# Optimization experiments

Measured on AMD Instinct MI355X. Metric: run time of the kernel, lower is better.

## Reference

```python
import math
import jax, jax.numpy as jnp
import numpy as np


def positionalencoding1d(d_model, length):
    # [length, d_model]; d_model must be even
    position = jnp.arange(length, dtype=jnp.float32)[:, None]
    div_term = jnp.exp(jnp.arange(0, d_model, 2, dtype=jnp.float32) * (-(math.log(10000.0) / d_model)))
    pe = jnp.zeros((length, d_model), dtype=jnp.float32)
    pe = pe.at[:, 0::2].set(jnp.sin(position * div_term))
    pe = pe.at[:, 1::2].set(jnp.cos(position * div_term))
    return pe


def setup_inputs() -> dict:
    key = jax.random.key(0)
    k1, k2, k3 = jax.random.split(key, 3)
    B, D, H, W = 64, 512, 32, 32
    NH = 8
    DH = D // NH
    x = jax.random.normal(k1, (B, D, H, W), dtype=jnp.float32)
    q = jax.random.normal(k2, (1, NH, 1, DH), dtype=jnp.float32)
    Wkv = jax.random.normal(k3, (D, 2 * D), dtype=jnp.float32) * 0.02
    bkv = jnp.zeros((2 * D,), dtype=jnp.float32)
    return {"x": x, "q": q, "Wkv": Wkv, "bkv": bkv, "num_heads": NH}


def reference(x, q, Wkv, bkv, num_heads):
    B, d, h, w = x.shape
    N = h * w
    NH = num_heads
    DH = d // NH
    scale = DH ** (-0.5)

    xt = x.reshape(B, d, N).transpose(0, 2, 1)            # b n d
    kv = xt @ Wkv + bkv                                   # b n 2d
    k, v = jnp.split(kv, 2, axis=-1)
    k = k.reshape(B, N, NH, DH).transpose(0, 2, 1, 3)     # b h n d
    v = v.reshape(B, N, NH, DH).transpose(0, 2, 1, 3)     # b h n d

    pe = positionalencoding1d(DH, N)                      # n d, broadcast over b,h
    k = k + pe

    qh = q[0, :, 0, :]                                    # h d (shared learned query)
    dots = jnp.einsum('hd,bhnd->bhn', qh, k) * scale      # b h n
    attn = jax.nn.softmax(dots, axis=-1)
    out = jnp.einsum('bhn,bhnd->bhd', attn, v)            # b h d
    return out.reshape(B, NH * DH)                        # b (h d)
```

## Files before the change

kernel.cpp:

```cpp
#include <hip/hip_runtime.h>
#include <math.h>

#define BATCH  64
#define DCH    512
#define NPOS   1024
#define NH     8
#define NSPLIT 16
#define NRANGE 64

__global__ __launch_bounds__(256) void k_prep(const float* __restrict__ q,
                                              const float* __restrict__ Wkv,
                                              const float* __restrict__ bkv,
                                              float* __restrict__ wqT,
                                              float* __restrict__ bias) {
    int blk = blockIdx.x;
    if (blk < 2) {
        int c = blk * 256 + threadIdx.x;
        const float4* wrow = (const float4*)(Wkv + (size_t)c * (2 * DCH));
        const float4* q4   = (const float4*)q;
        #pragma unroll
        for (int h = 0; h < NH; ++h) {
            float s = 0.f;
            #pragma unroll
            for (int d4 = 0; d4 < 16; ++d4) {
                float4 a = q4[h * 16 + d4];
                float4 w = wrow[h * 16 + d4];
                s = fmaf(a.x, w.x, fmaf(a.y, w.y, fmaf(a.z, w.z, fmaf(a.w, w.w, s))));
            }
            wqT[c * NH + h] = 0.125f * s;
        }
    } else {
        int n = (blk - 2) * 256 + threadIdx.x;
        float pq[NH];
        #pragma unroll
        for (int h = 0; h < NH; ++h) pq[h] = 0.f;
        const float kfac2 = -13.2877123795494f / 64.f;
        for (int i = 0; i < 32; ++i) {
            float dt = exp2f((float)(2 * i) * kfac2);
            float ang = (float)n * dt;
            float sn, cs;
            sincosf(ang, &sn, &cs);
            #pragma unroll
            for (int h = 0; h < NH; ++h)
                pq[h] = fmaf(q[h * 64 + 2 * i], sn,
                        fmaf(q[h * 64 + 2 * i + 1], cs, pq[h]));
        }
        #pragma unroll
        for (int h = 0; h < NH; ++h) {
            float bq = 0.f;
            #pragma unroll 8
            for (int d = 0; d < 64; ++d)
                bq = fmaf(q[h * 64 + d], bkv[h * 64 + d], bq);
            bias[h * NPOS + n] = 0.125f * (pq[h] + bq);
        }
    }
}

__global__ __launch_bounds__(512, 4) void k_flash(const float* __restrict__ x,
                                                  const float* __restrict__ wqT,
                                                  const float* __restrict__ bias,
                                                  float* __restrict__ apart,
                                                  float* __restrict__ mz) {
    __shared__ float wqs[DCH * NH];
    __shared__ float sred[8][NH][NRANGE];
    __shared__ float pbuf[NH][NRANGE];

    int b = blockIdx.y, ns = blockIdx.x;
    int t = threadIdx.x;
    int w = t >> 6;
    int lane = t & 63;
    int n0 = ns * NRANGE;
    int c0 = w * 64;

    {
        const float4* src = (const float4*)wqT;
        float4* dst = (float4*)wqs;
        #pragma unroll
        for (int i = 0; i < 2; ++i) dst[t + 512 * i] = src[t + 512 * i];
    }
    __syncthreads();

    {
        int rg = lane >> 4;
        int n4 = lane & 15;
        const float* xbase = x + ((size_t)b * DCH + c0 + rg) * NPOS + n0 + n4 * 4;

        float acc[NH][4];
        #pragma unroll
        for (int h = 0; h < NH; ++h)
            #pragma unroll
            for (int e = 0; e < 4; ++e) acc[h][e] = 0.f;

        #pragma unroll
        for (int g = 0; g < 2; ++g) {
            float4 xv[8];
            #pragma unroll
            for (int u = 0; u < 8; ++u)
                xv[u] = *(const float4*)(xbase + (size_t)(4 * (8 * g + u)) * NPOS);
            #pragma unroll
            for (int u = 0; u < 8; ++u) {
                int c = c0 + 4 * (8 * g + u) + rg;
                float wv[8];
                *(float4*)&wv[0] = *(const float4*)&wqs[c * 8];
                *(float4*)&wv[4] = *(const float4*)&wqs[c * 8 + 4];
                #pragma unroll
                for (int h = 0; h < NH; ++h) {
                    acc[h][0] = fmaf(xv[u].x, wv[h], acc[h][0]);
                    acc[h][1] = fmaf(xv[u].y, wv[h], acc[h][1]);
                    acc[h][2] = fmaf(xv[u].z, wv[h], acc[h][2]);
                    acc[h][3] = fmaf(xv[u].w, wv[h], acc[h][3]);
                }
            }
        }
        #pragma unroll
        for (int h = 0; h < NH; ++h)
            #pragma unroll
            for (int e = 0; e < 4; ++e) {
                float v = acc[h][e];
                v += __shfl_xor(v, 16);
                v += __shfl_xor(v, 32);
                acc[h][e] = v;
            }
        if (rg == 0) {
            #pragma unroll
            for (int h = 0; h < NH; ++h)
                *(float4*)&sred[w][h][n4 * 4] =
                    make_float4(acc[h][0], acc[h][1], acc[h][2], acc[h][3]);
        }
    }
    __syncthreads();

    {
        int h = w;
        int n = lane;
        float s = bias[h * NPOS + n0 + n];
        #pragma unroll
        for (int o = 0; o < 8; ++o) s += sred[o][h][n];
        float m = s;
        #pragma unroll
        for (int o = 32; o; o >>= 1) m = fmaxf(m, __shfl_xor(m, o));
        float p = expf(s - m);
        float z = p;
        #pragma unroll
        for (int o = 32; o; o >>= 1) z += __shfl_xor(z, o);
        pbuf[h][n] = p;
        if (lane == 0) {
            float* mzp = mz + ((size_t)ns * BATCH + b) * 2 * NH;
            mzp[h]      = m;
            mzp[NH + h] = z;
        }
    }
    __syncthreads();

    {
        int rg = lane >> 2;
        int nq = lane & 3;
        const float* xb3 = x + ((size_t)b * DCH + c0 + rg) * NPOS + n0 + nq * 4;

        float con[4][NH];
        #pragma unroll
        for (int p = 0; p < 4; ++p)
            #pragma unroll
            for (int h = 0; h < NH; ++h) con[p][h] = 0.f;

        float4 xcur[4], xnxt[4];
        #pragma unroll
        for (int p = 0; p < 4; ++p)
            xcur[p] = *(const float4*)(xb3 + (size_t)(p * 16) * NPOS);

        #pragma unroll
        for (int j = 0; j < 4; ++j) {
            if (j < 3) {
                #pragma unroll
                for (int p = 0; p < 4; ++p)
                    xnxt[p] = *(const float4*)(xb3 + (size_t)(p * 16) * NPOS + (j + 1) * 16);
            }
            float4 pj[NH];
            #pragma unroll
            for (int h = 0; h < NH; ++h)
                pj[h] = *(const float4*)&pbuf[h][j * 16 + nq * 4];
            #pragma unroll
            for (int p = 0; p < 4; ++p) {
                #pragma unroll
                for (int h = 0; h < NH; ++h)
                    con[p][h] = fmaf(xcur[p].x, pj[h].x, fmaf(xcur[p].y, pj[h].y,
                                fmaf(xcur[p].z, pj[h].z, fmaf(xcur[p].w, pj[h].w, con[p][h]))));
            }
            #pragma unroll
            for (int p = 0; p < 4; ++p) xcur[p] = xnxt[p];
        }

        #pragma unroll
        for (int p = 0; p < 4; ++p)
            #pragma unroll
            for (int h = 0; h < NH; ++h) {
                float v = con[p][h];
                v += __shfl_xor(v, 1);
                v += __shfl_xor(v, 2);
                con[p][h] = v;
            }

        size_t abase = ((size_t)ns * BATCH + b) * (NH * DCH);
        #pragma unroll
        for (int p = 0; p < 4; ++p) {
            int c = c0 + p * 16 + rg;
            float lo = (nq == 0) ? con[p][0] : (nq == 1) ? con[p][1]
                     : (nq == 2) ? con[p][2] : con[p][3];
            float hi = (nq == 0) ? con[p][4] : (nq == 1) ? con[p][5]
                     : (nq == 2) ? con[p][6] : con[p][7];
            apart[abase + (size_t)nq * DCH + c]       = lo;
            apart[abase + (size_t)(nq + 4) * DCH + c] = hi;
        }
    }
}

__global__ __launch_bounds__(512) void k_comb(const float* __restrict__ apart,
                                              const float* __restrict__ mz,
                                              const float* __restrict__ Wkv,
                                              const float* __restrict__ bkv,
                                              float* __restrict__ out) {
    __shared__ float as[NH * DCH];
    __shared__ float red[2][256];
    int b = blockIdx.x, half = blockIdx.y, t = threadIdx.x;
    int h = t >> 6;

    float M = -1e30f;
    #pragma unroll
    for (int j = 0; j < NSPLIT; ++j)
        M = fmaxf(M, mz[((size_t)j * BATCH + b) * 2 * NH + h]);
    float Z = 0.f, fj[NSPLIT];
    #pragma unroll
    for (int j = 0; j < NSPLIT; ++j) {
        const float* mzp = mz + ((size_t)j * BATCH + b) * 2 * NH;
        fj[j] = expf(mzp[h] - M);
        Z = fmaf(fj[j], mzp[NH + h], Z);
    }
    float invZ = 1.f / Z;

    int e0 = t * 8;
    float v[8];
    #pragma unroll
    for (int k = 0; k < 8; ++k) v[k] = 0.f;
    #pragma unroll
    for (int j = 0; j < NSPLIT; ++j) {
        const float* src = apart + ((size_t)j * BATCH + b) * (NH * DCH) + e0;
        float4 lo = *(const float4*)(src);
        float4 hi = *(const float4*)(src + 4);
        v[0] = fmaf(fj[j], lo.x, v[0]);
        v[1] = fmaf(fj[j], lo.y, v[1]);
        v[2] = fmaf(fj[j], lo.z, v[2]);
        v[3] = fmaf(fj[j], lo.w, v[3]);
        v[4] = fmaf(fj[j], hi.x, v[4]);
        v[5] = fmaf(fj[j], hi.y, v[5]);
        v[6] = fmaf(fj[j], hi.z, v[6]);
        v[7] = fmaf(fj[j], hi.w, v[7]);
    }
    #pragma unroll
    for (int k = 0; k < 8; ++k) as[e0 + k] = v[k] * invZ;
    __syncthreads();

    int o  = t & 255;
    int cp = t >> 8;
    int hd = half * 256 + o;
    int ho = hd >> 6;
    float a0 = 0.f, a1 = 0.f, a2 = 0.f, a3 = 0.f;
    const float* wp  = Wkv + DCH + hd;
    const float* apr = as + ho * DCH;
    int cbeg = cp * 256;
    #pragma unroll 4
    for (int c = cbeg; c < cbeg + 256; c += 4) {
        a0 = fmaf(apr[c],     wp[(size_t)c * (2 * DCH)],       a0);
        a1 = fmaf(apr[c + 1], wp[(size_t)(c + 1) * (2 * DCH)], a1);
        a2 = fmaf(apr[c + 2], wp[(size_t)(c + 2) * (2 * DCH)], a2);
        a3 = fmaf(apr[c + 3], wp[(size_t)(c + 3) * (2 * DCH)], a3);
    }
    red[cp][o] = (a0 + a1) + (a2 + a3);
    __syncthreads();
    if (t < 256) {
        int hd2 = half * 256 + t;
        out[(size_t)b * DCH + hd2] = bkv[DCH + hd2] + red[0][t] + red[1][t];
    }
}

extern "C" void kernel_launch(void* const* d_in, const int* in_sizes, int n_in,
                              void* d_out, int out_size, void* d_ws, size_t ws_size,
                              hipStream_t stream) {
    const float* x   = (const float*)d_in[0];
    const float* q   = (const float*)d_in[1];
    const float* Wkv = (const float*)d_in[2];
    const float* bkv = (const float*)d_in[3];
    float* out = (float*)d_out;

    float* ws    = (float*)d_ws;
    float* wqT   = ws;
    float* bias  = wqT + DCH * NH;
    float* apart = bias + NH * NPOS;
    float* mz    = apart + (size_t)NSPLIT * BATCH * NH * DCH;

    hipLaunchKernelGGL(k_prep,  dim3(6),             dim3(256), 0, stream, q, Wkv, bkv, wqT, bias);
    hipLaunchKernelGGL(k_flash, dim3(NSPLIT, BATCH), dim3(512), 0, stream, x, wqT, bias, apart, mz);
    hipLaunchKernelGGL(k_comb,  dim3(BATCH, 2),      dim3(512), 0, stream, apart, mz, Wkv, bkv, out);
}
```

Measured before the change: 84.48 us.

## Stage x tile in LDS to avoid second global read; halve position range

The flash kernel now loads each block's x slice from global memory once, keeps it in a swizzled shared-memory tile, and reuses it for the weighted-V accumulation instead of re-reading x from global memory. The position range per block is halved (NRANGE 32, NSPLIT 32) so the tile fits in shared memory, which doubles the number of partial results the combine kernel must reduce. The combine loop unroll is reduced to limit register pressure. Shared memory use rises to about 80KB per block, which lowers occupancy, and the partial buffer traffic doubles.

```diff
diff --git a/kernel.cpp b/kernel.cpp
--- a/kernel.cpp
+++ b/kernel.cpp
@@ -5,8 +5,8 @@
 #define DCH    512
 #define NPOS   1024
 #define NH     8
-#define NSPLIT 16
-#define NRANGE 64
+#define NSPLIT 32
+#define NRANGE 32
 
 __global__ __launch_bounds__(256) void k_prep(const float* __restrict__ q,
                                               const float* __restrict__ Wkv,
@@ -56,14 +56,13 @@
     }
 }
 
-__global__ __launch_bounds__(512, 4) void k_flash(const float* __restrict__ x,
-                                                  const float* __restrict__ wqT,
-                                                  const float* __restrict__ bias,
-                                                  float* __restrict__ apart,
-                                                  float* __restrict__ mz) {
-    __shared__ float wqs[DCH * NH];
-    __shared__ float sred[8][NH][NRANGE];
-    __shared__ float pbuf[NH][NRANGE];
+__global__ __launch_bounds__(512) void k_flash(const float* __restrict__ x,
+                                               const float* __restrict__ wqT,
+                                               const float* __restrict__ bias,
+                                               float* __restrict__ apart,
+                                               float* __restrict__ mz) {
+    __shared__ float tile[DCH * NRANGE];
+    __shared__ float aux[4096];
 
     int b = blockIdx.y, ns = blockIdx.x;
     int t = threadIdx.x;
@@ -74,16 +73,20 @@
 
     {
         const float4* src = (const float4*)wqT;
-        float4* dst = (float4*)wqs;
-        #pragma unroll
-        for (int i = 0; i < 2; ++i) dst[t + 512 * i] = src[t + 512 * i];
-    }
-    __syncthreads();
-
+        float4* dst = (float4*)aux;
+        dst[t]       = src[t];
+        dst[t + 512] = src[t + 512];
+    }
+    __syncthreads();
+
+    int rg = lane >> 3;
+    int n8 = lane & 7;
     {
-        int rg = lane >> 4;
-        int n4 = lane & 15;
-        const float* xbase = x + ((size_t)b * DCH + c0 + rg) * NPOS + n0 + n4 * 4;
+        const float* gx = x + ((size_t)b * DCH + c0 + rg) * NPOS + n0 + n8 * 4;
+        float4 xv[8];
+        #pragma unroll
+        for (int k = 0; k < 8; ++k)
+            xv[k] = *(const float4*)(gx + (size_t)(8 * k) * NPOS);
 
         float acc[NH][4];
         #pragma unroll
@@ -92,24 +95,18 @@
             for (int e = 0; e < 4; ++e) acc[h][e] = 0.f;
 
         #pragma unroll
-        for (int g = 0; g < 2; ++g) {
-            float4 xv[8];
-            #pragma unroll
-            for (int u = 0; u < 8; ++u)
-                xv[u] = *(const float4*)(xbase + (size_t)(4 * (8 * g + u)) * NPOS);
-            #pragma unroll
-            for (int u = 0; u < 8; ++u) {
-                int c = c0 + 4 * (8 * g + u) + rg;
-                float wv[8];
-                *(float4*)&wv[0] = *(const float4*)&wqs[c * 8];
-                *(float4*)&wv[4] = *(const float4*)&wqs[c * 8 + 4];
-                #pragma unroll
-                for (int h = 0; h < NH; ++h) {
-                    acc[h][0] = fmaf(xv[u].x, wv[h], acc[h][0]);
-                    acc[h][1] = fmaf(xv[u].y, wv[h], acc[h][1]);
-                    acc[h][2] = fmaf(xv[u].z, wv[h], acc[h][2]);
-                    acc[h][3] = fmaf(xv[u].w, wv[h], acc[h][3]);
-                }
+        for (int k = 0; k < 8; ++k) {
+            int c = c0 + 8 * k + rg;
+            *(float4*)&tile[c * NRANGE + ((n8 ^ rg) << 2)] = xv[k];
+            float wv[8];
+            *(float4*)&wv[0] = *(const float4*)&aux[c * 8];
+            *(float4*)&wv[4] = *(const float4*)&aux[c * 8 + 4];
+            #pragma unroll
+            for (int h = 0; h < NH; ++h) {
+                acc[h][0] = fmaf(xv[k].x, wv[h], acc[h][0]);
+                acc[h][1] = fmaf(xv[k].y, wv[h], acc[h][1]);
+                acc[h][2] = fmaf(xv[k].z, wv[h], acc[h][2]);
+                acc[h][3] = fmaf(xv[k].w, wv[h], acc[h][3]);
             }
         }
         #pragma unroll
@@ -117,33 +114,35 @@
             #pragma unroll
             for (int e = 0; e < 4; ++e) {
                 float v = acc[h][e];
+                v += __shfl_xor(v, 8);
                 v += __shfl_xor(v, 16);
                 v += __shfl_xor(v, 32);
                 acc[h][e] = v;
             }
+        __syncthreads();
         if (rg == 0) {
             #pragma unroll
             for (int h = 0; h < NH; ++h)
-                *(float4*)&sred[w][h][n4 * 4] =
+                *(float4*)&aux[(w * NH + h) * NRANGE + n8 * 4] =
                     make_float4(acc[h][0], acc[h][1], acc[h][2], acc[h][3]);
         }
     }
     __syncthreads();
 
-    {
+    if (lane < 32) {
         int h = w;
         int n = lane;
         float s = bias[h * NPOS + n0 + n];
         #pragma unroll
-        for (int o = 0; o < 8; ++o) s += sred[o][h][n];
+        for (int o = 0; o < 8; ++o) s += aux[(o * NH + h) * NRANGE + n];
         float m = s;
         #pragma unroll
-        for (int o = 32; o; o >>= 1) m = fmaxf(m, __shfl_xor(m, o));
+        for (int o = 16; o; o >>= 1) m = fmaxf(m, __shfl_xor(m, o));
         float p = expf(s - m);
         float z = p;
         #pragma unroll
-        for (int o = 32; o; o >>= 1) z += __shfl_xor(z, o);
-        pbuf[h][n] = p;
+        for (int o = 16; o; o >>= 1) z += __shfl_xor(z, o);
+        aux[2048 + h * NRANGE + n] = p;
         if (lane == 0) {
             float* mzp = mz + ((size_t)ns * BATCH + b) * 2 * NH;
             mzp[h]      = m;
@@ -153,9 +152,8 @@
     __syncthreads();
 
     {
-        int rg = lane >> 2;
-        int nq = lane & 3;
-        const float* xb3 = x + ((size_t)b * DCH + c0 + rg) * NPOS + n0 + nq * 4;
+        int rg16 = lane >> 2;
+        int nq   = lane & 3;
 
         float con[4][NH];
         #pragma unroll
@@ -163,31 +161,22 @@
             #pragma unroll
             for (int h = 0; h < NH; ++h) con[p][h] = 0.f;
 
-        float4 xcur[4], xnxt[4];
-        #pragma unroll
-        for (int p = 0; p < 4; ++p)
-            xcur[p] = *(const float4*)(xb3 + (size_t)(p * 16) * NPOS);
-
-        #pragma unroll
-        for (int j = 0; j < 4; ++j) {
-            if (j < 3) {
-                #pragma unroll
-                for (int p = 0; p < 4; ++p)
-                    xnxt[p] = *(const float4*)(xb3 + (size_t)(p * 16) * NPOS + (j + 1) * 16);
-            }
+        #pragma unroll
+        for (int j = 0; j < 2; ++j) {
             float4 pj[NH];
             #pragma unroll
             for (int h = 0; h < NH; ++h)
-                pj[h] = *(const float4*)&pbuf[h][j * 16 + nq * 4];
+                pj[h] = *(const float4*)&aux[2048 + h * NRANGE + nq * 4 + j * 16];
             #pragma unroll
             for (int p = 0; p < 4; ++p) {
+                int c = c0 + p * 16 + rg16;
+                int g = (nq + 4 * j) ^ (rg16 & 7);
+                float4 xr = *(const float4*)&tile[c * NRANGE + g * 4];
                 #pragma unroll
                 for (int h = 0; h < NH; ++h)
-                    con[p][h] = fmaf(xcur[p].x, pj[h].x, fmaf(xcur[p].y, pj[h].y,
-                                fmaf(xcur[p].z, pj[h].z, fmaf(xcur[p].w, pj[h].w, con[p][h]))));
-            }
-            #pragma unroll
-            for (int p = 0; p < 4; ++p) xcur[p] = xnxt[p];
+                    con[p][h] = fmaf(xr.x, pj[h].x, fmaf(xr.y, pj[h].y,
+                                fmaf(xr.z, pj[h].z, fmaf(xr.w, pj[h].w, con[p][h]))));
+            }
         }
 
         #pragma unroll
@@ -203,7 +192,7 @@
         size_t abase = ((size_t)ns * BATCH + b) * (NH * DCH);
         #pragma unroll
         for (int p = 0; p < 4; ++p) {
-            int c = c0 + p * 16 + rg;
+            int c = c0 + p * 16 + rg16;
             float lo = (nq == 0) ? con[p][0] : (nq == 1) ? con[p][1]
                      : (nq == 2) ? con[p][2] : con[p][3];
             float hi = (nq == 0) ? con[p][4] : (nq == 1) ? con[p][5]
@@ -241,7 +230,7 @@
     float v[8];
     #pragma unroll
     for (int k = 0; k < 8; ++k) v[k] = 0.f;
-    #pragma unroll
+    #pragma unroll 4
     for (int j = 0; j < NSPLIT; ++j) {
         const float* src = apart + ((size_t)j * BATCH + b) * (NH * DCH) + e0;
         float4 lo = *(const float4*)(src);
```

New measurement: 96.27 us. +14.0%, slower.
